# Kernel optimization log

Measured on AMD Instinct MI355X. Metric: run time of the kernel, lower is better.

The kernel has to match this reference:

```python
import jax, jax.numpy as jnp
import numpy as np

N_NODES = 50000
N_GRAPHS = 64
HIDDEN = 128
INPUT = 128
NEG_SLOPE = 0.2


def _gat_layer(x, src, dst, W, a_src, a_dst, b, n_nodes):
    # x: [N, Fin]; src/dst: [E] (self-loops already included)
    h = x @ W                              # [N, H]
    alpha_s = h @ a_src                    # [N]
    alpha_d = h @ a_dst                    # [N]
    e = alpha_s[src] + alpha_d[dst]        # [E]
    e = jnp.where(e > 0, e, NEG_SLOPE * e)  # leaky_relu(0.2)
    # segment softmax over destination node
    m = jax.ops.segment_max(e, dst, num_segments=n_nodes)  # [N]
    m = jnp.where(jnp.isfinite(m), m, 0.0)
    ee = jnp.exp(e - m[dst])
    s = jax.ops.segment_sum(ee, dst, num_segments=n_nodes)
    coef = ee / (s[dst] + 1e-16)           # [E]
    out = jax.ops.segment_sum(h[src] * coef[:, None], dst, num_segments=n_nodes)
    return out + b


def setup_inputs() -> dict:
    key = jax.random.key(0)
    ks = jax.random.split(key, 16)
    x = jax.random.normal(ks[0], (N_NODES, INPUT), dtype=jnp.float32)
    edge_index = jax.random.randint(ks[1], (2, 600000), 0, N_NODES, dtype=jnp.int64 if jax.config.x64_enabled else jnp.int32).astype(jnp.int32)
    batch = jnp.sort(jax.random.randint(ks[2], (N_NODES,), 0, N_GRAPHS)).astype(jnp.int32)
    def glorot(k, shape):
        lim = float(np.sqrt(6.0 / (shape[0] + shape[-1])))
        return jax.random.uniform(k, shape, jnp.float32, -lim, lim)
    params = {}
    dims = [(INPUT, HIDDEN), (HIDDEN, HIDDEN), (HIDDEN, HIDDEN)]
    for i, (fi, fo) in enumerate(dims, 1):
        params[f"W{i}"] = glorot(ks[3 * i], (fi, fo))
        params[f"a_src{i}"] = glorot(ks[3 * i + 1], (fo,)) * 0.1
        params[f"a_dst{i}"] = glorot(ks[3 * i + 2], (fo,)) * 0.1
        params[f"b{i}"] = jnp.zeros((fo,), jnp.float32)
    return dict(x=x, edge_index=edge_index, batch=batch, **params)


def reference(x, edge_index, batch,
              W1, a_src1, a_dst1, b1,
              W2, a_src2, a_dst2, b2,
              W3, a_src3, a_dst3, b3):
    n = x.shape[0]
    loops = jnp.arange(n, dtype=edge_index.dtype)
    src = jnp.concatenate([edge_index[0], loops])  # PyG add_self_loops=True
    dst = jnp.concatenate([edge_index[1], loops])
    h = jax.nn.elu(_gat_layer(x, src, dst, W1, a_src1, a_dst1, b1, n))
    h = jax.nn.elu(_gat_layer(h, src, dst, W2, a_src2, a_dst2, b2, n))
    h = jax.nn.elu(_gat_layer(h, src, dst, W3, a_src3, a_dst3, b3, n))
    # global_mean_pool
    sums = jax.ops.segment_sum(h, batch, num_segments=N_GRAPHS)
    cnt = jax.ops.segment_sum(jnp.ones((n,), h.dtype), batch, num_segments=N_GRAPHS)
    return sums / jnp.maximum(cnt, 1.0)[:, None]
```

## Files before the change

kernel.cpp:

```cpp
#include <hip/hip_runtime.h>
#include <math.h>

#define N_NODES 50000
#define N_GRAPHS 64
#define HID 128
#define SCAN_B 196
#define NODE_BLKS 196
#define NBUCK 128

typedef _Float16 half8 __attribute__((ext_vector_type(8)));
typedef float f32x4 __attribute__((ext_vector_type(4)));
typedef int i32x4 __attribute__((ext_vector_type(4)));

__device__ __forceinline__ float lrelu(float e) { return e > 0.f ? e : 0.2f * e; }
__device__ __forceinline__ float elu_fast(float o) { return o > 0.f ? o : __expf(o) - 1.f; }

__device__ __forceinline__ void fmix_lo(float& a, int h2, float c) {
    asm("v_fma_mix_f32 %0, %1, %2, %0 op_sel_hi:[1,0,0]" : "+v"(a) : "v"(h2), "v"(c));
}
__device__ __forceinline__ void fmix_hi(float& a, int h2, float c) {
    asm("v_fma_mix_f32 %0, %1, %2, %0 op_sel:[1,0,0] op_sel_hi:[1,0,0]" : "+v"(a) : "v"(h2), "v"(c));
}

__global__ void count_prep(const int* __restrict__ dst, int n_e, int nblk,
                           int* __restrict__ counts, int* __restrict__ start,
                           int* __restrict__ dhist, int* __restrict__ gcur,
                           const float* __restrict__ W0, const float* __restrict__ W1,
                           const float* __restrict__ W2,
                           const float* __restrict__ as0, const float* __restrict__ ad0,
                           const float* __restrict__ as1, const float* __restrict__ ad1,
                           const float* __restrict__ as2, const float* __restrict__ ad2,
                           _Float16* __restrict__ Wh0, _Float16* __restrict__ Wh1,
                           _Float16* __restrict__ Wh2,
                           float* __restrict__ wfold) {
    int blk = blockIdx.x;
    if (blk < nblk) {
        if (blk == 0) {
            if (threadIdx.x <= N_GRAPHS) start[threadIdx.x] = -1;
            if (threadIdx.x < NBUCK) { dhist[threadIdx.x] = 0; gcur[threadIdx.x] = 0; }
        }
        int e = blk * 256 + threadIdx.x;
        if (e < n_e) atomicAdd(&counts[dst[e]], 1);
        return;
    }
    int b = blk - nblk;
    if (b < 24) {
        int layer = b >> 3;
        const float* W = layer == 0 ? W0 : (layer == 1 ? W1 : W2);
        _Float16* Wh = layer == 0 ? Wh0 : (layer == 1 ? Wh1 : Wh2);
        int t = (b & 7) * 256 + threadIdx.x;
        int lane = t & 63;
        int nt = (t >> 6) & 7;
        int kt = t >> 9;
        int n = nt * 16 + (lane & 15);
        int kbase = kt * 32 + (lane >> 4) * 8;
#pragma unroll
        for (int j = 0; j < 8; ++j) {
            float w = W[(size_t)(kbase + j) * 128 + n];
            Wh[(size_t)t * 8 + j] = (_Float16)w;
        }
    } else {
        int idx = b - 24;
        int layer = idx >> 1, which = idx & 1;
        const float* W = layer == 0 ? W0 : (layer == 1 ? W1 : W2);
        const float* a = which == 0 ? (layer == 0 ? as0 : (layer == 1 ? as1 : as2))
                                    : (layer == 0 ? ad0 : (layer == 1 ? ad1 : ad2));
        int k = threadIdx.x;
        if (k < 128) {
            float s = 0.f;
            for (int j = 0; j < 128; ++j) s = fmaf(W[k * 128 + j], a[j], s);
            wfold[idx * 128 + k] = s;
        }
    }
}

__global__ __launch_bounds__(256) void block_reduce(const int* __restrict__ counts,
                                                    int* __restrict__ bsum) {
    __shared__ int red[256];
    int t = threadIdx.x;
    int i = blockIdx.x * 256 + t;
    red[t] = (i < N_NODES) ? counts[i] : 0;
    __syncthreads();
#pragma unroll
    for (int off = 128; off; off >>= 1) {
        if (t < off) red[t] += red[t + off];
        __syncthreads();
    }
    if (t == 0) bsum[blockIdx.x] = red[0];
}

__global__ __launch_bounds__(256) void block_scan(const int* __restrict__ counts,
                                                  const int* __restrict__ bsum,
                                                  const int* __restrict__ batch,
                                                  int* __restrict__ offs,
                                                  int* __restrict__ cursor,
                                                  int* __restrict__ start,
                                                  int* __restrict__ dhist) {
    __shared__ int sb[256];
    __shared__ int sh[256];
    __shared__ int lh[NBUCK];
    int t = threadIdx.x;
    if (t < NBUCK) lh[t] = 0;
    int v = (t < SCAN_B) ? bsum[t] : 0;
    sb[t] = v;
    __syncthreads();
#pragma unroll
    for (int off = 1; off < 256; off <<= 1) {
        int u = (t >= off) ? sb[t - off] : 0;
        __syncthreads();
        sb[t] += u;
        __syncthreads();
    }
    int bpre = (blockIdx.x == 0) ? 0 : sb[blockIdx.x - 1];
    if (blockIdx.x == 0 && t == SCAN_B - 1) offs[N_NODES] = sb[t];

    int i = blockIdx.x * 256 + t;
    int c = (i < N_NODES) ? counts[i] : 0;
    sh[t] = c;
    __syncthreads();
#pragma unroll
    for (int off = 1; off < 256; off <<= 1) {
        int u = (t >= off) ? sh[t - off] : 0;
        __syncthreads();
        sh[t] += u;
        __syncthreads();
    }
    if (i < N_NODES) {
        int e = bpre + sh[t] - c;
        offs[i] = e;
        cursor[i] = e;
        int b = batch[i];
        if (i == 0) start[b] = 0;
        else if (batch[i - 1] != b) start[b] = i;
        atomicAdd(&lh[c < NBUCK - 1 ? c : NBUCK - 1], 1);
    }
    __syncthreads();
    if (t < NBUCK) {
        int n = lh[t];
        if (n) atomicAdd(&dhist[t], n);
    }
}

__global__ __launch_bounds__(256) void scatter_kernel(const int* __restrict__ src,
                                                      const int* __restrict__ dst, int n_e,
                                                      int* __restrict__ cursor,
                                                      int* __restrict__ csr_src,
                                                      float* __restrict__ outz,
                                                      const int* __restrict__ offs,
                                                      const int* __restrict__ dhist,
                                                      int* __restrict__ gcur,
                                                      int* __restrict__ order) {
    int gid = blockIdx.x * 256 + threadIdx.x;
    if (gid < N_GRAPHS * HID) outz[gid] = 0.f;
    if (gid < n_e) {
        int d = dst[gid];
        int pos = atomicAdd(&cursor[d], 1);
        csr_src[pos] = src[gid];
    }
    if (blockIdx.x >= NODE_BLKS) return;

    __shared__ int lh[NBUCK], sc[NBUCK], lbase[NBUCK];
    int t = threadIdx.x;
    if (t < NBUCK) lh[t] = 0;
    __syncthreads();
    int b = -1, lpos = 0;
    if (gid < N_NODES) {
        int deg = offs[gid + 1] - offs[gid];
        b = deg < NBUCK - 1 ? deg : NBUCK - 1;
        lpos = atomicAdd(&lh[b], 1);
    }
    __syncthreads();
    if (t < NBUCK) sc[t] = dhist[t];
    __syncthreads();
    for (int off = 1; off < NBUCK; off <<= 1) {
        int u = (t < NBUCK && t >= off) ? sc[t - off] : 0;
        __syncthreads();
        if (t < NBUCK) sc[t] += u;
        __syncthreads();
    }
    if (t < NBUCK) {
        int excl = t ? sc[t - 1] : 0;
        int cnt = lh[t];
        int bb = cnt ? atomicAdd(&gcur[t], cnt) : 0;
        lbase[t] = excl + bb;
    }
    __syncthreads();
    if (gid < N_NODES) order[lbase[b] + lpos] = gid;
}

__global__ __launch_bounds__(256) void gemm_mfma(const float* __restrict__ X,
                                                 const _Float16* __restrict__ Wh,
                                                 const float* __restrict__ wsv,
                                                 const float* __restrict__ wdv,
                                                 _Float16* __restrict__ H16,
                                                 float* __restrict__ AS,
                                                 float* __restrict__ AD) {
    __shared__ float wsL[128], wdL[128];
    int t = threadIdx.x;
    if (t < 128) wsL[t] = wsv[t];
    else if (t < 256) wdL[t - 128] = wdv[t - 128];
    __syncthreads();

    int wave = t >> 6, lane = t & 63;
    int m15 = lane & 15, quad = lane >> 4;
    int rowbase = blockIdx.x * 64 + wave * 16;
    int arow = rowbase + m15;
    bool arow_ok = arow < N_NODES;

    f32x4 acc[8];
#pragma unroll
    for (int nt = 0; nt < 8; ++nt) acc[nt] = (f32x4){0.f, 0.f, 0.f, 0.f};
    float as_p = 0.f, ad_p = 0.f;

    const float* xrow = X + (size_t)arow * 128 + quad * 8;
#pragma unroll
    for (int kt = 0; kt < 4; ++kt) {
        f32x4 a0 = (f32x4){0.f, 0.f, 0.f, 0.f};
        f32x4 a1 = (f32x4){0.f, 0.f, 0.f, 0.f};
        if (arow_ok) {
            a0 = *(const f32x4*)(xrow + kt * 32);
            a1 = *(const f32x4*)(xrow + kt * 32 + 4);
        }
        int kb = kt * 32 + quad * 8;
        half8 ah;
#pragma unroll
        for (int j = 0; j < 4; ++j) {
            as_p = fmaf(a0[j], wsL[kb + j], as_p);
            ad_p = fmaf(a0[j], wdL[kb + j], ad_p);
            as_p = fmaf(a1[j], wsL[kb + 4 + j], as_p);
            ad_p = fmaf(a1[j], wdL[kb + 4 + j], ad_p);
            ah[j] = (_Float16)a0[j];
            ah[4 + j] = (_Float16)a1[j];
        }
#pragma unroll
        for (int nt = 0; nt < 8; ++nt) {
            size_t fidx = ((size_t)((kt * 8 + nt) * 64 + lane)) * 8;
            half8 bh = *(const half8*)(Wh + fidx);
            acc[nt] = __builtin_amdgcn_mfma_f32_16x16x32_f16(ah, bh, acc[nt], 0, 0, 0);
        }
    }

#pragma unroll
    for (int nt = 0; nt < 8; ++nt) {
        int c = nt * 16 + m15;
#pragma unroll
        for (int reg = 0; reg < 4; ++reg) {
            int gr = rowbase + quad * 4 + reg;
            if (gr < N_NODES) H16[(size_t)gr * 128 + c] = (_Float16)acc[nt][reg];
        }
    }
    as_p += __shfl_xor(as_p, 16);
    ad_p += __shfl_xor(ad_p, 16);
    as_p += __shfl_xor(as_p, 32);
    ad_p += __shfl_xor(ad_p, 32);
    if (quad == 0 && arow_ok) { AS[arow] = as_p; AD[arow] = ad_p; }
}

__global__ __launch_bounds__(256) void aggregate_kernel(const _Float16* __restrict__ H16,
                                                        const float* __restrict__ AS,
                                                        const float* __restrict__ AD,
                                                        const int* __restrict__ offs,
                                                        const int* __restrict__ csr_src,
                                                        const int* __restrict__ order,
                                                        const float* __restrict__ bias,
                                                        float* __restrict__ OUT) {
    __shared__ int2 sh_sp[16][64];
    int tid = threadIdx.x;
    int quad = tid >> 4;
    int l16 = tid & 15;
    int node = order[blockIdx.x * 16 + quad];

    int beg = offs[node];
    int deg = offs[node + 1] - beg;
    float ad = AD[node];
    float eself = lrelu(AS[node] + ad);
    const i32x4* H4 = (const i32x4*)H16;
    i32x4 hsv = H4[(size_t)node * 16 + l16];
    bool fast = deg <= 64;

    float m, ssum = 0.f, ps;
    if (fast) {
        float mym = -INFINITY;
        for (int i = l16; i < deg; i += 16) {
            int sv = csr_src[beg + i];
            float e = lrelu(AS[sv] + ad);
            sh_sp[quad][i] = make_int2(sv, __float_as_int(e));
            mym = fmaxf(mym, e);
        }
#pragma unroll
        for (int off = 8; off; off >>= 1) mym = fmaxf(mym, __shfl_xor(mym, off, 16));
        m = fmaxf(mym, eself);
        ps = __expf(eself - m);
        for (int i = l16; i < deg; i += 16) {
            int2 sp = sh_sp[quad][i];
            float p = __expf(__int_as_float(sp.y) - m);
            sh_sp[quad][i] = make_int2(sp.x, __float_as_int(p));
            ssum += p;
        }
    } else {
        float mym = -INFINITY;
        for (int i = beg + l16; i < beg + deg; i += 16)
            mym = fmaxf(mym, lrelu(AS[csr_src[i]] + ad));
#pragma unroll
        for (int off = 8; off; off >>= 1) mym = fmaxf(mym, __shfl_xor(mym, off, 16));
        m = fmaxf(mym, eself);
        ps = __expf(eself - m);
        for (int i = beg + l16; i < beg + deg; i += 16)
            ssum += __expf(lrelu(AS[csr_src[i]] + ad) - m);
    }

    float accA[8] = {0.f, 0.f, 0.f, 0.f, 0.f, 0.f, 0.f, 0.f};
    float accB[8] = {0.f, 0.f, 0.f, 0.f, 0.f, 0.f, 0.f, 0.f};

    if (fast) {
        int k = 0;
        for (; k + 3 < deg; k += 4) {
            int2 sp0 = sh_sp[quad][k];
            int2 sp1 = sh_sp[quad][k + 1];
            int2 sp2 = sh_sp[quad][k + 2];
            int2 sp3 = sh_sp[quad][k + 3];
            i32x4 h0 = H4[(size_t)sp0.x * 16 + l16];
            i32x4 h1 = H4[(size_t)sp1.x * 16 + l16];
            i32x4 h2 = H4[(size_t)sp2.x * 16 + l16];
            i32x4 h3 = H4[(size_t)sp3.x * 16 + l16];
            float c0 = __int_as_float(sp0.y), c1 = __int_as_float(sp1.y);
            float c2 = __int_as_float(sp2.y), c3 = __int_as_float(sp3.y);
#pragma unroll
            for (int j = 0; j < 4; ++j) {
                fmix_lo(accA[2 * j], h0[j], c0);
                fmix_hi(accA[2 * j + 1], h0[j], c0);
                fmix_lo(accB[2 * j], h1[j], c1);
                fmix_hi(accB[2 * j + 1], h1[j], c1);
            }
#pragma unroll
            for (int j = 0; j < 4; ++j) {
                fmix_lo(accA[2 * j], h2[j], c2);
                fmix_hi(accA[2 * j + 1], h2[j], c2);
                fmix_lo(accB[2 * j], h3[j], c3);
                fmix_hi(accB[2 * j + 1], h3[j], c3);
            }
        }
        for (; k < deg; ++k) {
            int2 sp0 = sh_sp[quad][k];
            float c0 = __int_as_float(sp0.y);
            i32x4 h0 = H4[(size_t)sp0.x * 16 + l16];
#pragma unroll
            for (int j = 0; j < 4; ++j) {
                fmix_lo(accA[2 * j], h0[j], c0);
                fmix_hi(accA[2 * j + 1], h0[j], c0);
            }
        }
    } else {
        for (int k = 0; k < deg; ++k) {
            int s = csr_src[beg + k];
            float c = __expf(lrelu(AS[s] + ad) - m);
            i32x4 h0 = H4[(size_t)s * 16 + l16];
#pragma unroll
            for (int j = 0; j < 4; ++j) {
                fmix_lo(accA[2 * j], h0[j], c);
                fmix_hi(accA[2 * j + 1], h0[j], c);
            }
        }
    }

#pragma unroll
    for (int j = 0; j < 4; ++j) {
        fmix_lo(accA[2 * j], hsv[j], ps);
        fmix_hi(accA[2 * j + 1], hsv[j], ps);
    }
#pragma unroll
    for (int off = 8; off; off >>= 1) ssum += __shfl_xor(ssum, off, 16);
    float inv = __builtin_amdgcn_rcpf(ssum + ps + 1e-16f);

    f32x4 b0 = ((const f32x4*)bias)[l16 * 2];
    f32x4 b1 = ((const f32x4*)bias)[l16 * 2 + 1];
    f32x4 o0, o1;
    o0.x = elu_fast(fmaf(accA[0] + accB[0], inv, b0.x));
    o0.y = elu_fast(fmaf(accA[1] + accB[1], inv, b0.y));
    o0.z = elu_fast(fmaf(accA[2] + accB[2], inv, b0.z));
    o0.w = elu_fast(fmaf(accA[3] + accB[3], inv, b0.w));
    o1.x = elu_fast(fmaf(accA[4] + accB[4], inv, b1.x));
    o1.y = elu_fast(fmaf(accA[5] + accB[5], inv, b1.y));
    o1.z = elu_fast(fmaf(accA[6] + accB[6], inv, b1.z));
    o1.w = elu_fast(fmaf(accA[7] + accB[7], inv, b1.w));
    ((f32x4*)OUT)[(size_t)node * 32 + l16 * 2] = o0;
    ((f32x4*)OUT)[(size_t)node * 32 + l16 * 2 + 1] = o1;
}

__device__ __forceinline__ int estart(const int* __restrict__ start, int g) {
    for (; g < N_GRAPHS; ++g) {
        int v = start[g];
        if (v >= 0) return v;
    }
    return N_NODES;
}

__global__ __launch_bounds__(128) void pool_kernel(const float* __restrict__ F,
                                                   const int* __restrict__ start,
                                                   float* __restrict__ out) {
    int b = blockIdx.x;
    int g = b >> 4, sub = b & 15;
    int c = threadIdx.x;
    int s0 = estart(start, g), e0 = estart(start, g + 1);
    float acc = 0.f;
    for (int i = s0 + sub; i < e0; i += 16) acc += F[(size_t)i * 128 + c];
    int cnt = e0 - s0;
    float r = 1.f / (float)(cnt > 1 ? cnt : 1);
    atomicAdd(&out[(size_t)g * 128 + c], acc * r);
}

extern "C" void kernel_launch(void* const* d_in, const int* in_sizes, int n_in,
                              void* d_out, int out_size, void* d_ws, size_t ws_size,
                              hipStream_t stream) {
    const float* x = (const float*)d_in[0];
    const int* edge_index = (const int*)d_in[1];
    const int* batch = (const int*)d_in[2];
    const float* W[3]   = {(const float*)d_in[3], (const float*)d_in[7], (const float*)d_in[11]};
    const float* avs[3] = {(const float*)d_in[4], (const float*)d_in[8], (const float*)d_in[12]};
    const float* avd[3] = {(const float*)d_in[5], (const float*)d_in[9], (const float*)d_in[13]};
    const float* bb[3]  = {(const float*)d_in[6], (const float*)d_in[10], (const float*)d_in[14]};
    int E0 = in_sizes[1] / 2;
    const int* esrc = edge_index;
    const int* edst = edge_index + E0;

    char* p = (char*)d_ws;
    auto alloc = [&](size_t bytes) -> void* {
        void* q = (void*)p;
        p += (bytes + 255) & ~(size_t)255;
        return q;
    };
    int* counts   = (int*)alloc((size_t)N_NODES * 4);
    int* offs     = (int*)alloc((size_t)(N_NODES + 1) * 4);
    int* cursor   = (int*)alloc((size_t)N_NODES * 4);
    int* csr_src  = (int*)alloc((size_t)E0 * 4);
    int* start    = (int*)alloc((N_GRAPHS + 1) * 4);
    int* bsum     = (int*)alloc(SCAN_B * 4);
    int* dhist    = (int*)alloc(NBUCK * 4);
    int* gcur     = (int*)alloc(NBUCK * 4);
    int* order    = (int*)alloc((size_t)N_NODES * 4);
    float* AS     = (float*)alloc((size_t)N_NODES * 4);
    float* AD     = (float*)alloc((size_t)N_NODES * 4);
    float* wfold  = (float*)alloc(6 * 128 * 4);
    _Float16* H16 = (_Float16*)alloc((size_t)N_NODES * HID * 2);
    float* FA     = (float*)alloc((size_t)N_NODES * HID * 4);
    float* FB     = (float*)alloc((size_t)N_NODES * HID * 4);
    _Float16* Wh[3];
    for (int l = 0; l < 3; ++l) Wh[l] = (_Float16*)alloc(16384 * 2);

    int nblk = (E0 + 255) / 256;
    hipMemsetAsync(counts, 0, (size_t)N_NODES * 4, stream);
    count_prep<<<nblk + 30, 256, 0, stream>>>(edst, E0, nblk, counts, start, dhist, gcur,
                                              W[0], W[1], W[2], avs[0], avd[0], avs[1], avd[1],
                                              avs[2], avd[2], Wh[0], Wh[1], Wh[2], wfold);
    block_reduce<<<SCAN_B, 256, 0, stream>>>(counts, bsum);
    block_scan<<<SCAN_B, 256, 0, stream>>>(counts, bsum, batch, offs, cursor, start, dhist);
    scatter_kernel<<<nblk, 256, 0, stream>>>(esrc, edst, E0, cursor, csr_src, (float*)d_out,
                                             offs, dhist, gcur, order);

    const float* cur = x;
    float* feat[2] = {FA, FB};
    for (int l = 0; l < 3; ++l) {
        gemm_mfma<<<(N_NODES + 63) / 64, 256, 0, stream>>>(cur, Wh[l],
                                                           wfold + (l * 2) * 128,
                                                           wfold + (l * 2 + 1) * 128,
                                                           H16, AS, AD);
        float* nxt = feat[l & 1];
        aggregate_kernel<<<N_NODES / 16, 256, 0, stream>>>(H16, AS, AD, offs, csr_src, order,
                                                           bb[l], nxt);
        cur = nxt;
    }

    pool_kernel<<<N_GRAPHS * 16, 128, 0, stream>>>(cur, start, (float*)d_out);
}
```

Measured before the change: 305.2 us.

## Fuse next layer's GEMM and attention projections into aggregate kernel epilogue

```diff
diff --git a/kernel.cpp b/kernel.cpp
--- a/kernel.cpp
+++ b/kernel.cpp
@@ -7,6 +7,7 @@
 #define SCAN_B 196
 #define NODE_BLKS 196
 #define NBUCK 128
+#define AP 132
 
 typedef _Float16 half8 __attribute__((ext_vector_type(8)));
 typedef float f32x4 __attribute__((ext_vector_type(4)));
@@ -263,8 +264,15 @@
                                                         const int* __restrict__ csr_src,
                                                         const int* __restrict__ order,
                                                         const float* __restrict__ bias,
+                                                        const _Float16* __restrict__ Whn,
+                                                        const float* __restrict__ wfn,
+                                                        _Float16* __restrict__ Hn,
+                                                        float* __restrict__ ASn,
+                                                        float* __restrict__ ADn,
                                                         float* __restrict__ OUT) {
     __shared__ int2 sh_sp[16][64];
+    __shared__ _Float16 aW[16][AP];
+    __shared__ int nds[16];
     int tid = threadIdx.x;
     int quad = tid >> 4;
     int l16 = tid & 15;
@@ -372,6 +380,7 @@
     for (int off = 8; off; off >>= 1) ssum += __shfl_xor(ssum, off, 16);
     float inv = __builtin_amdgcn_rcpf(ssum + ps + 1e-16f);
 
+    int c0i = l16 * 8;
     f32x4 b0 = ((const f32x4*)bias)[l16 * 2];
     f32x4 b1 = ((const f32x4*)bias)[l16 * 2 + 1];
     f32x4 o0, o1;
@@ -383,8 +392,57 @@
     o1.y = elu_fast(fmaf(accA[5] + accB[5], inv, b1.y));
     o1.z = elu_fast(fmaf(accA[6] + accB[6], inv, b1.z));
     o1.w = elu_fast(fmaf(accA[7] + accB[7], inv, b1.w));
-    ((f32x4*)OUT)[(size_t)node * 32 + l16 * 2] = o0;
-    ((f32x4*)OUT)[(size_t)node * 32 + l16 * 2 + 1] = o1;
+    if (OUT) {
+        ((f32x4*)OUT)[(size_t)node * 32 + l16 * 2] = o0;
+        ((f32x4*)OUT)[(size_t)node * 32 + l16 * 2 + 1] = o1;
+    }
+
+    if (Whn) {
+        const float* wsn = wfn;
+        const float* wdn = wfn + 128;
+        float asn = o0.x * wsn[c0i] + o0.y * wsn[c0i + 1] + o0.z * wsn[c0i + 2] +
+                    o0.w * wsn[c0i + 3] + o1.x * wsn[c0i + 4] + o1.y * wsn[c0i + 5] +
+                    o1.z * wsn[c0i + 6] + o1.w * wsn[c0i + 7];
+        float adn = o0.x * wdn[c0i] + o0.y * wdn[c0i + 1] + o0.z * wdn[c0i + 2] +
+                    o0.w * wdn[c0i + 3] + o1.x * wdn[c0i + 4] + o1.y * wdn[c0i + 5] +
+                    o1.z * wdn[c0i + 6] + o1.w * wdn[c0i + 7];
+#pragma unroll
+        for (int off = 8; off; off >>= 1) {
+            asn += __shfl_xor(asn, off, 16);
+            adn += __shfl_xor(adn, off, 16);
+        }
+        if (l16 == 0) {
+            ASn[node] = asn;
+            ADn[node] = adn;
+            nds[quad] = node;
+        }
+        half8 hh;
+        hh[0] = (_Float16)o0.x; hh[1] = (_Float16)o0.y;
+        hh[2] = (_Float16)o0.z; hh[3] = (_Float16)o0.w;
+        hh[4] = (_Float16)o1.x; hh[5] = (_Float16)o1.y;
+        hh[6] = (_Float16)o1.z; hh[7] = (_Float16)o1.w;
+        *(half8*)&aW[quad][c0i] = hh;
+        __syncthreads();
+
+        int wv = tid >> 6, lane = tid & 63;
+        int m15 = lane & 15, eq = lane >> 4;
+        f32x4 acc0 = (f32x4){0.f, 0.f, 0.f, 0.f};
+        f32x4 acc1 = (f32x4){0.f, 0.f, 0.f, 0.f};
+#pragma unroll
+        for (int kt = 0; kt < 4; ++kt) {
+            half8 ah = *(const half8*)&aW[m15][kt * 32 + eq * 8];
+            half8 bh0 = *(const half8*)(Whn + ((size_t)((kt * 8 + wv * 2) * 64 + lane)) * 8);
+            half8 bh1 = *(const half8*)(Whn + ((size_t)((kt * 8 + wv * 2 + 1) * 64 + lane)) * 8);
+            acc0 = __builtin_amdgcn_mfma_f32_16x16x32_f16(ah, bh0, acc0, 0, 0, 0);
+            acc1 = __builtin_amdgcn_mfma_f32_16x16x32_f16(ah, bh1, acc1, 0, 0, 0);
+        }
+#pragma unroll
+        for (int reg = 0; reg < 4; ++reg) {
+            int nid = nds[eq * 4 + reg];
+            Hn[(size_t)nid * 128 + wv * 32 + m15] = (_Float16)acc0[reg];
+            Hn[(size_t)nid * 128 + wv * 32 + 16 + m15] = (_Float16)acc1[reg];
+        }
+    }
 }
 
 __device__ __forceinline__ int estart(const int* __restrict__ start, int g) {
@@ -438,12 +496,14 @@
     int* dhist    = (int*)alloc(NBUCK * 4);
     int* gcur     = (int*)alloc(NBUCK * 4);
     int* order    = (int*)alloc((size_t)N_NODES * 4);
-    float* AS     = (float*)alloc((size_t)N_NODES * 4);
-    float* AD     = (float*)alloc((size_t)N_NODES * 4);
+    float* ASa    = (float*)alloc((size_t)N_NODES * 4);
+    float* ADa    = (float*)alloc((size_t)N_NODES * 4);
+    float* ASb    = (float*)alloc((size_t)N_NODES * 4);
+    float* ADb    = (float*)alloc((size_t)N_NODES * 4);
     float* wfold  = (float*)alloc(6 * 128 * 4);
-    _Float16* H16 = (_Float16*)alloc((size_t)N_NODES * HID * 2);
+    _Float16* Ha  = (_Float16*)alloc((size_t)N_NODES * HID * 2);
+    _Float16* Hb  = (_Float16*)alloc((size_t)N_NODES * HID * 2);
     float* FA     = (float*)alloc((size_t)N_NODES * HID * 4);
-    float* FB     = (float*)alloc((size_t)N_NODES * HID * 4);
     _Float16* Wh[3];
     for (int l = 0; l < 3; ++l) Wh[l] = (_Float16*)alloc(16384 * 2);
 
@@ -457,18 +517,17 @@
     scatter_kernel<<<nblk, 256, 0, stream>>>(esrc, edst, E0, cursor, csr_src, (float*)d_out,
                                              offs, dhist, gcur, order);
 
-    const float* cur = x;
-    float* feat[2] = {FA, FB};
-    for (int l = 0; l < 3; ++l) {
-        gemm_mfma<<<(N_NODES + 63) / 64, 256, 0, stream>>>(cur, Wh[l],
-                                                           wfold + (l * 2) * 128,
-                                                           wfold + (l * 2 + 1) * 128,
-                                                           H16, AS, AD);
-        float* nxt = feat[l & 1];
-        aggregate_kernel<<<N_NODES / 16, 256, 0, stream>>>(H16, AS, AD, offs, csr_src, order,
-                                                           bb[l], nxt);
-        cur = nxt;
-    }
-
-    pool_kernel<<<N_GRAPHS * 16, 128, 0, stream>>>(cur, start, (float*)d_out);
-}
+    gemm_mfma<<<(N_NODES + 63) / 64, 256, 0, stream>>>(x, Wh[0], wfold, wfold + 128,
+                                                       Ha, ASa, ADa);
+    aggregate_kernel<<<N_NODES / 16, 256, 0, stream>>>(Ha, ASa, ADa, offs, csr_src, order,
+                                                       bb[0], Wh[1], wfold + 2 * 128,
+                                                       Hb, ASb, ADb, nullptr);
+    aggregate_kernel<<<N_NODES / 16, 256, 0, stream>>>(Hb, ASb, ADb, offs, csr_src, order,
+                                                       bb[1], Wh[2], wfold + 4 * 128,
+                                                       Ha, ASa, ADa, nullptr);
+    aggregate_kernel<<<N_NODES / 16, 256, 0, stream>>>(Ha, ASa, ADa, offs, csr_src, order,
+                                                       bb[2], nullptr, nullptr,
+                                                       nullptr, nullptr, nullptr, FA);
+
+    pool_kernel<<<N_GRAPHS * 16, 128, 0, stream>>>(FA, start, (float*)d_out);
+}
```

New measurement: 279.6 us. 1.09x faster.
